# Optimization experiments

Measured on AMD Instinct MI355X. Metric: run time of the kernel, lower is better.

## Reference

```python
import jax, jax.numpy as jnp
import numpy as np

H = 16
HD = 128
ROPE_BASE = 10000.0

def _rope_cos_sin(T, dtype):
    inv_freq = 1.0 / (ROPE_BASE ** (jnp.arange(0, HD, 2, dtype=jnp.float32) / HD))  # [HD/2]
    pos = jnp.arange(T, dtype=jnp.float32)
    freqs = pos[:, None] * inv_freq[None, :]  # [T, HD/2]
    return jnp.cos(freqs).astype(dtype), jnp.sin(freqs).astype(dtype)

def _apply_rotary(x, cos, sin):
    # x: [B,H,T,HD]; cos/sin: [T,HD/2]
    x1, x2 = x[..., : HD // 2], x[..., HD // 2 :]
    c = cos[None, None, :, :]
    s = sin[None, None, :, :]
    return jnp.concatenate([x1 * c - x2 * s, x1 * s + x2 * c], axis=-1)

def setup_inputs() -> dict:
    key = jax.random.key(0)
    ks = jax.random.split(key, 5)
    B, T, D = 2, 2048, 2048
    x = jax.random.normal(ks[0], (B, T, D), dtype=jnp.float32)
    Wqkv = jax.random.normal(ks[1], (3 * D, D), dtype=jnp.float32) * (D ** -0.5)
    bqkv = jax.random.normal(ks[2], (3 * D,), dtype=jnp.float32) * 0.02
    Wo = jax.random.normal(ks[3], (D, D), dtype=jnp.float32) * (D ** -0.5)
    bo = jax.random.normal(ks[4], (D,), dtype=jnp.float32) * 0.02
    # causal mask: True = masked (future positions)
    mask = jnp.triu(jnp.ones((T, T), dtype=bool), k=1)[None, None, :, :]
    return {"x": x, "Wqkv": Wqkv, "bqkv": bqkv, "Wo": Wo, "bo": bo, "mask": mask}

def reference(x, Wqkv, bqkv, Wo, bo, mask):
    B, T, D = x.shape
    qkv = x @ Wqkv.T + bqkv  # [B,T,3D]
    q, k, v = jnp.split(qkv, 3, axis=-1)
    def to_heads(t):
        return t.reshape(B, T, H, HD).transpose(0, 2, 1, 3)  # [B,H,T,HD]
    q, k, v = to_heads(q), to_heads(k), to_heads(v)
    cos, sin = _rope_cos_sin(T, x.dtype)
    q = _apply_rotary(q, cos, sin)
    k = _apply_rotary(k, cos, sin)
    scale = HD ** 0.5
    attn = jnp.einsum('bhqd,bhkd->bhqk', q, k) / scale
    neg = -jnp.finfo(x.dtype).max
    attn = jnp.where(mask, neg, attn)
    w = jax.nn.softmax(attn, axis=-1)
    out = jnp.einsum('bhqk,bhkd->bhqd', w, v)  # [B,H,T,HD]
    out = out.transpose(0, 2, 1, 3).reshape(B, T, H * HD)
    return out @ Wo.T + bo
```

## Files before the change

kernel.cpp:

```cpp
#include <hip/hip_runtime.h>
#include <hip/hip_bf16.h>
#include <cstdint>

typedef __bf16 bf16;
typedef __bf16 bf16x8 __attribute__((ext_vector_type(8)));
typedef float  f32x4  __attribute__((ext_vector_type(4)));

#define B_   2
#define T_   2048
#define D_   2048
#define H_   16
#define HD_  128

typedef __attribute__((address_space(3))) void       lds_void;
typedef __attribute__((address_space(1))) const void gbl_void;
__device__ __forceinline__ void glds16(const bf16* g, bf16* l) {
    __builtin_amdgcn_global_load_lds((gbl_void*)g, (lds_void*)l, 16, 0, 0);
}

__device__ __forceinline__ ushort4 cvt4(const float4 v) {
    union { bf16 h[4]; ushort4 u; } pk;
    pk.h[0] = (bf16)v.x; pk.h[1] = (bf16)v.y;
    pk.h[2] = (bf16)v.z; pk.h[3] = (bf16)v.w;
    return pk.u;
}

__global__ __launch_bounds__(256) void convert_xw_kernel(
    const float* __restrict__ x, const float* __restrict__ wqkv,
    bf16* __restrict__ xb, bf16* __restrict__ wqkvb)
{
    const int NX = (B_ * T_ * D_) / 4;
    const int NT = NX + (3 * D_ * D_) / 4;
    for (int g = blockIdx.x * blockDim.x + threadIdx.x; g < NT;
         g += gridDim.x * blockDim.x) {
        if (g < NX) ((ushort4*)xb)[g]      = cvt4(((const float4*)x)[g]);
        else        ((ushort4*)wqkvb)[g-NX] = cvt4(((const float4*)wqkv)[g-NX]);
    }
}

__global__ __launch_bounds__(256) void convert_wo_kernel(
    const float* __restrict__ wo, bf16* __restrict__ wob)
{
    const int N = (D_ * D_) / 4;
    for (int g = blockIdx.x * blockDim.x + threadIdx.x; g < N;
         g += gridDim.x * blockDim.x)
        ((ushort4*)wob)[g] = cvt4(((const float4*)wo)[g]);
}

__device__ __forceinline__ void gemm_core_glds(
    const bf16* __restrict__ A, const bf16* __restrict__ W, int K,
    int bm, int bn, int tid, f32x4 (&acc)[4][4],
    bf16* lds_a, bf16* lds_b)
{
    const int lane = tid & 63, quad = lane >> 4, lcol = lane & 15;
    const int wave = tid >> 6;
    const int wm = (wave >> 1) * 64, wn2 = (wave & 1) * 32;
    const int sw = lcol & 7;
    const int sr = tid >> 3, pc = tid & 7;
    const int sc = (pc ^ (sr & 7)) * 8;
    const bf16* abase = A + (size_t)(bm * 128 + sr) * K + sc;
    const bf16* bbase = W + (size_t)(bn * 128 + sr) * K + sc;
    bf16* la = lds_a + sr * 64 + pc * 8;
    bf16* lb = lds_b + sr * 64 + pc * 8;

    for (int k0 = 0; k0 < K; k0 += 64) {
        __syncthreads();
#pragma unroll
        for (int p = 0; p < 4; p++) {
            glds16(abase + k0 + (size_t)32 * p * K, la + 2048 * p);
            glds16(bbase + k0 + (size_t)32 * p * K, lb + 2048 * p);
        }
        __syncthreads();
#pragma unroll
        for (int kk = 0; kk < 2; kk++) {
            bf16x8 af[4], bfr[4];
#pragma unroll
            for (int i = 0; i < 4; i++)
                af[i] = *(const bf16x8*)&lds_a[(wm + i * 16 + lcol) * 64 +
                                               (((kk * 4 + quad) ^ sw) * 8)];
#pragma unroll
            for (int j = 0; j < 4; j++) {
                const int row = wn2 + (j & 1) * 16 + (j >> 1) * 64 + lcol;
                bfr[j] = *(const bf16x8*)&lds_b[row * 64 +
                                                (((kk * 4 + quad) ^ sw) * 8)];
            }
#pragma unroll
            for (int i = 0; i < 4; i++)
#pragma unroll
                for (int j = 0; j < 4; j++)
                    acc[i][j] = __builtin_amdgcn_mfma_f32_16x16x32_bf16(af[i], bfr[j], acc[i][j], 0, 0, 0);
        }
    }
}

__global__ __launch_bounds__(256) void qkv_gemm_kernel(
    const bf16* __restrict__ xb, const bf16* __restrict__ wqkvb,
    const float* __restrict__ bias,
    bf16* __restrict__ qh, bf16* __restrict__ kh, bf16* __restrict__ vT)
{
    __shared__ bf16 lds_a[128 * 64];
    __shared__ bf16 lds_b[128 * 64];
    const int tid = threadIdx.x;
    const int bm = blockIdx.y, bn = blockIdx.x;
    const int lane = tid & 63, quad = lane >> 4, lcol = lane & 15;
    const int wave = tid >> 6;
    const int wm = (wave >> 1) * 64, wn2 = (wave & 1) * 32;

    f32x4 acc[4][4];
    const f32x4 z = {0.f, 0.f, 0.f, 0.f};
#pragma unroll
    for (int i = 0; i < 4; i++)
#pragma unroll
        for (int j = 0; j < 4; j++) acc[i][j] = z;

    gemm_core_glds(xb, wqkvb, D_, bm, bn, tid, acc, lds_a, lds_b);

    const int n0 = bn * 128;
    const int part = bn / 16;
    const int h = bn & 15;
    const int mb0 = bm * 128 + wm;

    if (part < 2) {
        bf16* dst = (part == 0) ? qh : kh;
#pragma unroll
        for (int i = 0; i < 4; i++) {
#pragma unroll
            for (int jp = 0; jp < 2; jp++) {
                const int d1 = wn2 + jp * 16 + lcol;
                const float invf = __expf(-0.14391156831212787f * (float)d1);
                const float b1 = bias[n0 + d1];
                const float b2 = bias[n0 + d1 + 64];
#pragma unroll
                for (int r = 0; r < 4; r++) {
                    const int m = mb0 + i * 16 + quad * 4 + r;
                    const int bb = m >> 11, t = m & (T_ - 1);
                    const float x1 = acc[i][jp][r] + b1;
                    const float x2 = acc[i][jp + 2][r] + b2;
                    float s, c;
                    __sincosf((float)t * invf, &s, &c);
                    const size_t rowo = ((size_t)(bb * H_ + h) * T_ + t) * HD_;
                    dst[rowo + d1]      = (bf16)(x1 * c - x2 * s);
                    dst[rowo + d1 + 64] = (bf16)(x1 * s + x2 * c);
                }
            }
        }
    } else {
#pragma unroll
        for (int i = 0; i < 4; i++) {
            const int m4 = mb0 + i * 16 + quad * 4;
            const int bb = m4 >> 11, t4 = m4 & (T_ - 1);
            const int bh = bb * H_ + h;
#pragma unroll
            for (int j = 0; j < 4; j++) {
                const int d = wn2 + (j & 1) * 16 + (j >> 1) * 64 + lcol;
                const float bv = bias[n0 + d];
                union { bf16 hh[4]; ushort4 u; } pk;
#pragma unroll
                for (int r = 0; r < 4; r++) pk.hh[r] = (bf16)(acc[i][j][r] + bv);
                *(ushort4*)&vT[((size_t)bh * HD_ + d) * T_ + t4] = pk.u;
            }
        }
    }
}

__global__ __launch_bounds__(256) void attn_kernel(
    const bf16* __restrict__ qh, const bf16* __restrict__ kh,
    const bf16* __restrict__ vT, bf16* __restrict__ ctx)
{
    __shared__ bf16 lds_p[128][72];
    const int tid = threadIdx.x;
    const int id = blockIdx.x;
    const int bh = id & 31;
    const int q5 = (id >> 5) & 7;
    const int qt = (id >> 8) ? (15 - q5) : q5;
    const int q0 = qt * 128;
    const int lane = tid & 63, quad = lane >> 4, lcol = lane & 15;
    const int wave = tid >> 6;
    const int wq0 = wave * 32;
    const float scale2 = 0.08838834764831845f * 1.4426950408889634f;

    const bf16* kbase = kh + (size_t)bh * T_ * HD_;
    const bf16* vbase = vT + (size_t)bh * HD_ * T_;

    bf16x8 qf[2][4];
#pragma unroll
    for (int i = 0; i < 2; i++)
#pragma unroll
        for (int kk = 0; kk < 4; kk++)
            qf[i][kk] = *(const bf16x8*)&qh[((size_t)bh * T_ + q0 + wq0 + i * 16 + lcol) * HD_ + kk * 32 + quad * 8];

    f32x4 o[2][8];
    const f32x4 z = {0.f, 0.f, 0.f, 0.f};
#pragma unroll
    for (int i = 0; i < 2; i++)
#pragma unroll
        for (int jd = 0; jd < 8; jd++) o[i][jd] = z;
    float l_part[2][4];
#pragma unroll
    for (int i = 0; i < 2; i++)
#pragma unroll
        for (int r = 0; r < 4; r++) l_part[i][r] = 0.f;

    const int ktmax = ((q0 + wq0 + 31) >> 6) + 1;
    for (int kt = 0; kt < ktmax; kt++) {
        const bool diag = (kt == ktmax - 1);
        const bf16* krow = kbase + (size_t)(kt * 64) * HD_ + quad * 8;
        f32x4 s_acc[2][4];
#pragma unroll
        for (int i = 0; i < 2; i++)
#pragma unroll
            for (int j = 0; j < 4; j++) s_acc[i][j] = z;
#pragma unroll
        for (int kk = 0; kk < 4; kk++) {
            bf16x8 bk[4];
#pragma unroll
            for (int j = 0; j < 4; j++)
                bk[j] = *(const bf16x8*)&krow[(size_t)(j * 16 + lcol) * HD_ + kk * 32];
#pragma unroll
            for (int i = 0; i < 2; i++)
#pragma unroll
                for (int j = 0; j < 4; j++)
                    s_acc[i][j] = __builtin_amdgcn_mfma_f32_16x16x32_bf16(qf[i][kk], bk[j], s_acc[i][j], 0, 0, 0);
        }
#pragma unroll
        for (int i = 0; i < 2; i++) {
#pragma unroll
            for (int r = 0; r < 4; r++) {
                const int qrow = q0 + wq0 + i * 16 + quad * 4 + r;
                float lp = 0.f;
#pragma unroll
                for (int j = 0; j < 4; j++) {
                    float p = exp2f(fmaf(s_acc[i][j][r], scale2, -16.0f));
                    if (diag) {
                        const int kcol = kt * 64 + j * 16 + lcol;
                        p = (kcol > qrow) ? 0.f : p;
                    }
                    lp += p;
                    lds_p[wq0 + i * 16 + quad * 4 + r][j * 16 + lcol] = (bf16)p;
                }
                l_part[i][r] += lp;
            }
        }
        const bf16* vrow = vbase + kt * 64 + quad * 8;
#pragma unroll
        for (int kk2 = 0; kk2 < 2; kk2++) {
            bf16x8 pf[2], vf[8];
#pragma unroll
            for (int i = 0; i < 2; i++)
                pf[i] = *(const bf16x8*)&lds_p[wq0 + i * 16 + lcol][kk2 * 32 + quad * 8];
#pragma unroll
            for (int jd = 0; jd < 8; jd++)
                vf[jd] = *(const bf16x8*)&vrow[(size_t)(jd * 16 + lcol) * T_ + kk2 * 32];
#pragma unroll
            for (int i = 0; i < 2; i++)
#pragma unroll
                for (int jd = 0; jd < 8; jd++)
                    o[i][jd] = __builtin_amdgcn_mfma_f32_16x16x32_bf16(pf[i], vf[jd], o[i][jd], 0, 0, 0);
        }
    }
    float inv_l[2][4];
#pragma unroll
    for (int i = 0; i < 2; i++)
#pragma unroll
        for (int r = 0; r < 4; r++) {
            float rs = l_part[i][r];
#pragma unroll
            for (int off = 1; off < 16; off <<= 1)
                rs += __shfl_xor(rs, off);
            inv_l[i][r] = 1.0f / rs;
        }
    const int b = bh >> 4, h = bh & 15;
#pragma unroll
    for (int i = 0; i < 2; i++) {
#pragma unroll
        for (int r = 0; r < 4; r++) {
            const int t = q0 + wq0 + i * 16 + quad * 4 + r;
#pragma unroll
            for (int jd = 0; jd < 8; jd++)
                ctx[((size_t)(b * T_ + t)) * D_ + h * HD_ + jd * 16 + lcol] =
                    (bf16)(o[i][jd][r] * inv_l[i][r]);
        }
    }
}

__global__ __launch_bounds__(256) void proj_gemm_kernel(
    const bf16* __restrict__ ctx, const bf16* __restrict__ wob,
    const float* __restrict__ bias, float* __restrict__ out)
{
    __shared__ bf16 lds_a[128 * 64];
    __shared__ bf16 lds_b[128 * 64];
    const int tid = threadIdx.x;
    const int bm = blockIdx.y, bn = blockIdx.x;
    const int lane = tid & 63, quad = lane >> 4, lcol = lane & 15;
    const int wave = tid >> 6;
    const int wm = (wave >> 1) * 64, wn2 = (wave & 1) * 32;

    f32x4 acc[4][4];
    const f32x4 z = {0.f, 0.f, 0.f, 0.f};
#pragma unroll
    for (int i = 0; i < 4; i++)
#pragma unroll
        for (int j = 0; j < 4; j++) acc[i][j] = z;

    gemm_core_glds(ctx, wob, D_, bm, bn, tid, acc, lds_a, lds_b);

    const int n0 = bn * 128;
#pragma unroll
    for (int i = 0; i < 4; i++) {
#pragma unroll
        for (int j = 0; j < 4; j++) {
            const int n = n0 + wn2 + (j & 1) * 16 + (j >> 1) * 64 + lcol;
            const float bv = bias[n];
#pragma unroll
            for (int r = 0; r < 4; r++) {
                const int m = bm * 128 + wm + i * 16 + quad * 4 + r;
                out[(size_t)m * D_ + n] = acc[i][j][r] + bv;
            }
        }
    }
}

extern "C" void kernel_launch(void* const* d_in, const int* in_sizes, int n_in,
                              void* d_out, int out_size, void* d_ws, size_t ws_size,
                              hipStream_t stream)
{
    const float* x    = (const float*)d_in[0];
    const float* Wqkv = (const float*)d_in[1];
    const float* bqkv = (const float*)d_in[2];
    const float* Wo   = (const float*)d_in[3];
    const float* bo   = (const float*)d_in[4];
    float* out = (float*)d_out;

    const size_t HT = (size_t)B_ * H_ * T_ * HD_;
    bf16* xb   = (bf16*)d_ws;
    bf16* qh   = xb + HT;
    bf16* kh   = qh + HT;
    bf16* vT   = kh + HT;
    bf16* ctx  = xb;
    bf16* wob  = qh;
    bf16* wqkvb = (bf16*)d_out;

    convert_xw_kernel<<<2560, 256, 0, stream>>>(x, Wqkv, xb, wqkvb);
    qkv_gemm_kernel<<<dim3(48, 32), 256, 0, stream>>>(xb, wqkvb, bqkv, qh, kh, vT);
    attn_kernel<<<512, 256, 0, stream>>>(qh, kh, vT, ctx);
    convert_wo_kernel<<<1024, 256, 0, stream>>>(Wo, wob);
    proj_gemm_kernel<<<dim3(16, 32), 256, 0, stream>>>(ctx, wob, bo, out);
}
```

Before: 434.8 us.

## Stage K tiles in LDS with double buffering and shrink attention query tiles

The attention kernel now loads each 64-key K tile once per block into swizzled LDS using async global-to-LDS copies, double-buffered so the next tile's load overlaps compute. Previously every wave read K straight from global memory. Query tiles shrink to 64 rows (16 per wave) and the grid doubles to 1024 blocks, with s_setprio raised around the MFMA sections. The V-transpose store in the QKV GEMM and the P layout in LDS use a matching permutation of keys within each 64-block, so stores are wider without changing results. In exchange there are more blocks, each re-reading K/V for fewer queries, plus a barrier every key tile.

```diff
diff --git a/kernel.cpp b/kernel.cpp
--- a/kernel.cpp
+++ b/kernel.cpp
@@ -145,141 +145,147 @@
             }
         }
     } else {
-#pragma unroll
-        for (int i = 0; i < 4; i++) {
-            const int m4 = mb0 + i * 16 + quad * 4;
-            const int bb = m4 >> 11, t4 = m4 & (T_ - 1);
-            const int bh = bb * H_ + h;
-#pragma unroll
-            for (int j = 0; j < 4; j++) {
-                const int d = wn2 + (j & 1) * 16 + (j >> 1) * 64 + lcol;
-                const float bv = bias[n0 + d];
+        const int bb = mb0 >> 11, t64 = mb0 & (T_ - 1);
+        const int bh = bb * H_ + h;
+#pragma unroll
+        for (int j = 0; j < 4; j++) {
+            const int d = wn2 + (j & 1) * 16 + (j >> 1) * 64 + lcol;
+            const float bv = bias[n0 + d];
+            bf16* vdst = &vT[((size_t)bh * HD_ + d) * T_ + t64];
+#pragma unroll
+            for (int r = 0; r < 4; r++) {
                 union { bf16 hh[4]; ushort4 u; } pk;
 #pragma unroll
-                for (int r = 0; r < 4; r++) pk.hh[r] = (bf16)(acc[i][j][r] + bv);
-                *(ushort4*)&vT[((size_t)bh * HD_ + d) * T_ + t4] = pk.u;
-            }
-        }
-    }
-}
-
-__global__ __launch_bounds__(256) void attn_kernel(
+                for (int i = 0; i < 4; i++) pk.hh[i] = (bf16)(acc[i][j][r] + bv);
+                *(ushort4*)&vdst[(quad * 4 + r) * 4] = pk.u;
+            }
+        }
+    }
+}
+
+__global__ __launch_bounds__(256, 4) void attn_kernel(
     const bf16* __restrict__ qh, const bf16* __restrict__ kh,
     const bf16* __restrict__ vT, bf16* __restrict__ ctx)
 {
-    __shared__ bf16 lds_p[128][72];
+    __shared__ bf16 lds_k[2][64 * 128];
+    __shared__ bf16 lds_p[64 * 64];
     const int tid = threadIdx.x;
     const int id = blockIdx.x;
     const int bh = id & 31;
-    const int q5 = (id >> 5) & 7;
-    const int qt = (id >> 8) ? (15 - q5) : q5;
-    const int q0 = qt * 128;
+    const int q5 = (id >> 5) & 15;
+    const int qt = (id >> 9) ? (31 - q5) : q5;
+    const int q0 = qt * 64;
     const int lane = tid & 63, quad = lane >> 4, lcol = lane & 15;
     const int wave = tid >> 6;
-    const int wq0 = wave * 32;
+    const int wq0 = wave * 16;
     const float scale2 = 0.08838834764831845f * 1.4426950408889634f;
 
     const bf16* kbase = kh + (size_t)bh * T_ * HD_;
     const bf16* vbase = vT + (size_t)bh * HD_ * T_;
 
-    bf16x8 qf[2][4];
-#pragma unroll
-    for (int i = 0; i < 2; i++)
-#pragma unroll
-        for (int kk = 0; kk < 4; kk++)
-            qf[i][kk] = *(const bf16x8*)&qh[((size_t)bh * T_ + q0 + wq0 + i * 16 + lcol) * HD_ + kk * 32 + quad * 8];
-
-    f32x4 o[2][8];
+    const int srow = tid >> 4;
+    const int scol = ((tid & 15) ^ srow) << 3;
+    const bf16* kstage = kbase + (size_t)srow * HD_ + scol;
+
+    bf16x8 qf[4];
+#pragma unroll
+    for (int kk = 0; kk < 4; kk++)
+        qf[kk] = *(const bf16x8*)&qh[((size_t)bh * T_ + q0 + wq0 + lcol) * HD_ +
+                                     kk * 32 + quad * 8];
+
+    f32x4 o[8];
     const f32x4 z = {0.f, 0.f, 0.f, 0.f};
 #pragma unroll
-    for (int i = 0; i < 2; i++)
-#pragma unroll
-        for (int jd = 0; jd < 8; jd++) o[i][jd] = z;
-    float l_part[2][4];
-#pragma unroll
-    for (int i = 0; i < 2; i++)
-#pragma unroll
-        for (int r = 0; r < 4; r++) l_part[i][r] = 0.f;
-
-    const int ktmax = ((q0 + wq0 + 31) >> 6) + 1;
+    for (int jd = 0; jd < 8; jd++) o[jd] = z;
+    float l_part[4] = {0.f, 0.f, 0.f, 0.f};
+
+    const int ktmax = qt + 1;
+#pragma unroll
+    for (int p = 0; p < 4; p++)
+        glds16(kstage + (size_t)p * 16 * HD_, &lds_k[0][tid * 8 + p * 2048]);
+
     for (int kt = 0; kt < ktmax; kt++) {
-        const bool diag = (kt == ktmax - 1);
-        const bf16* krow = kbase + (size_t)(kt * 64) * HD_ + quad * 8;
-        f32x4 s_acc[2][4];
-#pragma unroll
-        for (int i = 0; i < 2; i++)
-#pragma unroll
-            for (int j = 0; j < 4; j++) s_acc[i][j] = z;
+        __syncthreads();
+        if (kt + 1 < ktmax) {
+            const bf16* ks = kstage + (size_t)(kt + 1) * 64 * HD_;
+#pragma unroll
+            for (int p = 0; p < 4; p++)
+                glds16(ks + (size_t)p * 16 * HD_,
+                       &lds_k[(kt + 1) & 1][tid * 8 + p * 2048]);
+        }
+        const bf16* lk = lds_k[kt & 1];
+
+        f32x4 s_acc[4];
+#pragma unroll
+        for (int j = 0; j < 4; j++) s_acc[j] = z;
+        __builtin_amdgcn_s_setprio(1);
 #pragma unroll
         for (int kk = 0; kk < 4; kk++) {
-            bf16x8 bk[4];
-#pragma unroll
-            for (int j = 0; j < 4; j++)
-                bk[j] = *(const bf16x8*)&krow[(size_t)(j * 16 + lcol) * HD_ + kk * 32];
-#pragma unroll
-            for (int i = 0; i < 2; i++)
-#pragma unroll
-                for (int j = 0; j < 4; j++)
-                    s_acc[i][j] = __builtin_amdgcn_mfma_f32_16x16x32_bf16(qf[i][kk], bk[j], s_acc[i][j], 0, 0, 0);
-        }
-#pragma unroll
-        for (int i = 0; i < 2; i++) {
-#pragma unroll
-            for (int r = 0; r < 4; r++) {
-                const int qrow = q0 + wq0 + i * 16 + quad * 4 + r;
-                float lp = 0.f;
-#pragma unroll
-                for (int j = 0; j < 4; j++) {
-                    float p = exp2f(fmaf(s_acc[i][j][r], scale2, -16.0f));
-                    if (diag) {
-                        const int kcol = kt * 64 + j * 16 + lcol;
-                        p = (kcol > qrow) ? 0.f : p;
-                    }
-                    lp += p;
-                    lds_p[wq0 + i * 16 + quad * 4 + r][j * 16 + lcol] = (bf16)p;
+#pragma unroll
+            for (int j = 0; j < 4; j++) {
+                const bf16x8 bk = *(const bf16x8*)&lk[(j * 16 + lcol) * 128 +
+                                        (((kk * 4 + quad) ^ lcol) << 3)];
+                s_acc[j] = __builtin_amdgcn_mfma_f32_16x16x32_bf16(qf[kk], bk, s_acc[j], 0, 0, 0);
+            }
+        }
+        __builtin_amdgcn_s_setprio(0);
+
+        const bool diag = (kt == qt);
+#pragma unroll
+        for (int r = 0; r < 4; r++) {
+            const int prow = wq0 + quad * 4 + r;
+            const int qrow = q0 + prow;
+            union { bf16 hh[4]; ushort4 u; } pk;
+            float lp = 0.f;
+#pragma unroll
+            for (int j = 0; j < 4; j++) {
+                float p = exp2f(fmaf(s_acc[j][r], scale2, -16.0f));
+                if (diag) {
+                    const int kcol = kt * 64 + j * 16 + lcol;
+                    p = (kcol > qrow) ? 0.f : p;
                 }
-                l_part[i][r] += lp;
-            }
-        }
+                lp += p;
+                pk.hh[j] = (bf16)p;
+            }
+            l_part[r] += lp;
+            *(ushort4*)&lds_p[prow * 64 + ((lcol * 4) ^ ((prow & 7) << 3))] = pk.u;
+        }
+
         const bf16* vrow = vbase + kt * 64 + quad * 8;
 #pragma unroll
         for (int kk2 = 0; kk2 < 2; kk2++) {
-            bf16x8 pf[2], vf[8];
-#pragma unroll
-            for (int i = 0; i < 2; i++)
-                pf[i] = *(const bf16x8*)&lds_p[wq0 + i * 16 + lcol][kk2 * 32 + quad * 8];
+            const int prow = wq0 + lcol;
+            const bf16x8 pf = *(const bf16x8*)&lds_p[prow * 64 +
+                                  ((kk2 * 32 + quad * 8) ^ ((lcol & 7) << 3))];
+            bf16x8 vf[8];
 #pragma unroll
             for (int jd = 0; jd < 8; jd++)
                 vf[jd] = *(const bf16x8*)&vrow[(size_t)(jd * 16 + lcol) * T_ + kk2 * 32];
-#pragma unroll
-            for (int i = 0; i < 2; i++)
-#pragma unroll
-                for (int jd = 0; jd < 8; jd++)
-                    o[i][jd] = __builtin_amdgcn_mfma_f32_16x16x32_bf16(pf[i], vf[jd], o[i][jd], 0, 0, 0);
-        }
-    }
-    float inv_l[2][4];
-#pragma unroll
-    for (int i = 0; i < 2; i++)
-#pragma unroll
-        for (int r = 0; r < 4; r++) {
-            float rs = l_part[i][r];
-#pragma unroll
-            for (int off = 1; off < 16; off <<= 1)
-                rs += __shfl_xor(rs, off);
-            inv_l[i][r] = 1.0f / rs;
-        }
+            __builtin_amdgcn_s_setprio(1);
+#pragma unroll
+            for (int jd = 0; jd < 8; jd++)
+                o[jd] = __builtin_amdgcn_mfma_f32_16x16x32_bf16(pf, vf[jd], o[jd], 0, 0, 0);
+            __builtin_amdgcn_s_setprio(0);
+        }
+    }
+
+    float inv_l[4];
+#pragma unroll
+    for (int r = 0; r < 4; r++) {
+        float rs = l_part[r];
+#pragma unroll
+        for (int off = 1; off < 16; off <<= 1)
+            rs += __shfl_xor(rs, off);
+        inv_l[r] = 1.0f / rs;
+    }
     const int b = bh >> 4, h = bh & 15;
 #pragma unroll
-    for (int i = 0; i < 2; i++) {
-#pragma unroll
-        for (int r = 0; r < 4; r++) {
-            const int t = q0 + wq0 + i * 16 + quad * 4 + r;
-#pragma unroll
-            for (int jd = 0; jd < 8; jd++)
-                ctx[((size_t)(b * T_ + t)) * D_ + h * HD_ + jd * 16 + lcol] =
-                    (bf16)(o[i][jd][r] * inv_l[i][r]);
-        }
+    for (int r = 0; r < 4; r++) {
+        const int t = q0 + wq0 + quad * 4 + r;
+#pragma unroll
+        for (int jd = 0; jd < 8; jd++)
+            ctx[((size_t)(b * T_ + t)) * D_ + h * HD_ + jd * 16 + lcol] =
+                (bf16)(o[jd][r] * inv_l[r]);
     }
 }
 
@@ -342,7 +348,7 @@
 
     convert_xw_kernel<<<2560, 256, 0, stream>>>(x, Wqkv, xb, wqkvb);
     qkv_gemm_kernel<<<dim3(48, 32), 256, 0, stream>>>(xb, wqkvb, bqkv, qh, kh, vT);
-    attn_kernel<<<512, 256, 0, stream>>>(qh, kh, vT, ctx);
+    attn_kernel<<<1024, 256, 0, stream>>>(qh, kh, vT, ctx);
     convert_wo_kernel<<<1024, 256, 0, stream>>>(Wo, wob);
     proj_gemm_kernel<<<dim3(16, 32), 256, 0, stream>>>(ctx, wob, bo, out);
 }
```

New measurement: 440.1 us. Within noise of the previous version (+1.2%).
